# Optimization experiments

Measured on AMD Instinct MI355X. Metric: run time of the kernel, lower is better.

Reference implementation:

```python
import jax, jax.numpy as jnp
import numpy as np

B, N, E, H = 2, 512, 128, 256
IN_DIM = 3 * E + 1


def setup_inputs() -> dict:
    key = jax.random.key(0)
    ks = jax.random.split(key, 9)
    node_embed = jax.random.normal(ks[0], (B, N, E), dtype=jnp.float32)
    problems = jax.random.uniform(ks[1], (B, N, 4), dtype=jnp.float32)
    euclid = jax.random.uniform(ks[2], (B, N, N), dtype=jnp.float32)
    euclid = 0.5 * (euclid + jnp.swapaxes(euclid, 1, 2))  # symmetric, realistic
    s = 0.02
    W1 = s * jax.random.normal(ks[3], (IN_DIM, H), dtype=jnp.float32)
    b1 = jnp.zeros((H,), jnp.float32)
    W2 = s * jax.random.normal(ks[4], (H, H), dtype=jnp.float32)
    b2 = jnp.zeros((H,), jnp.float32)
    W3 = s * jax.random.normal(ks[5], (H, 1), dtype=jnp.float32)
    b3 = jnp.zeros((1,), jnp.float32)
    return {"node_embed": node_embed, "problems": problems,
            "euclid_distance_matrix": euclid,
            "W1": W1, "b1": b1, "W2": W2, "b2": b2, "W3": W3, "b3": b3}


def _forward(node_embed, euclid, W1, b1, W2, b2, W3, b3):
    b, n, e = node_embed.shape
    hi = jnp.broadcast_to(node_embed[:, :, None, :], (b, n, n, e))
    hj = jnp.broadcast_to(node_embed[:, None, :, :], (b, n, n, e))
    habs = jnp.abs(node_embed[:, :, None, :] - node_embed[:, None, :, :])
    x = jnp.concatenate([hi, hj, habs, euclid[..., None]], axis=-1)  # (B,N,N,3E+1)
    h = jax.nn.relu(jnp.einsum('bijf,fh->bijh', x, W1) + b1)
    h = jax.nn.relu(jnp.einsum('bijh,hg->bijg', h, W2) + b2)
    pred = (jnp.einsum('bijh,ho->bijo', h, W3) + b3)[..., 0]  # (B,N,N)
    pred = 0.5 * (pred + jnp.swapaxes(pred, 1, 2))
    pred = pred * (1.0 - jnp.eye(n, dtype=pred.dtype))  # zero diagonal
    return pred


def reference(node_embed, problems, euclid_distance_matrix, W1, b1, W2, b2, W3, b3):
    # euclid_distance_matrix provided, so `problems` fallback path is unused
    return _forward(node_embed, euclid_distance_matrix, W1, b1, W2, b2, W3, b3)
```

## Files before the change

### kernel.cpp

```cpp
#include <hip/hip_runtime.h>
#include <hip/hip_bf16.h>


#define BN 512
#define EE 128
#define HH 256

typedef __attribute__((ext_vector_type(8)))  short short8;
typedef __attribute__((ext_vector_type(16))) float f32x16;
typedef __attribute__((ext_vector_type(4)))  float f32x4;

static __device__ __forceinline__ unsigned short f2bf(float f) {
    __bf16 h = (__bf16)f;
    return __builtin_bit_cast(unsigned short, h);
}
static __device__ __forceinline__ float bf2f(unsigned short s) {
    return (float)__builtin_bit_cast(__bf16, s);
}
static __device__ __forceinline__ f32x16 zero16() {
    f32x16 v;
    #pragma unroll
    for (int i = 0; i < 16; ++i) v[i] = 0.f;
    return v;
}
#define MFMA(a, b, c) __builtin_amdgcn_mfma_f32_32x32x16_bf16((a), (b), (c), 0, 0, 0)

__global__ void pack_all(const float* __restrict__ W1, const float* __restrict__ W2,
                         const float* __restrict__ b2,
                         unsigned short* __restrict__ w1c_p, unsigned short* __restrict__ w1b_p,
                         unsigned short* __restrict__ w2_p,  unsigned short* __restrict__ w1d_f,
                         unsigned short* __restrict__ b2_f) {
    int idx = blockIdx.x * 256 + threadIdx.x;
    {
        int t = idx & 7, l = (idx >> 3) & 63, nb = (idx >> 9) & 7, kb = idx >> 12;
        int k = kb * 16 + (l >> 5) * 8 + t, n = nb * 32 + (l & 31);
        w2_p[idx] = f2bf(W2[k * HH + n]);
        if (idx < 32768) {
            w1c_p[idx] = f2bf(W1[(2 * EE + k) * HH + n]);
            w1b_p[idx] = f2bf(W1[(EE + k) * HH + n]);
        }
    }
    if (idx < 4096) {
        int t = idx & 7, l = (idx >> 3) & 63, nb = idx >> 9;
        int n = nb * 32 + (l & 31);
        bool nz = (t == 0 && l < 32);
        w1d_f[idx] = nz ? f2bf(W1[(3 * EE) * HH + n]) : (unsigned short)0;
        b2_f[idx]  = nz ? f2bf(b2[n]) : (unsigned short)0;
    }
}

__global__ void precompute_pa(const float* __restrict__ node, const float* __restrict__ W1,
                              const float* __restrict__ b1, float* __restrict__ PA) {
    int bi = blockIdx.x, h = threadIdx.x;
    const float* nd = node + (size_t)bi * EE;
    float sa = b1[h];
    #pragma unroll 8
    for (int e = 0; e < EE; ++e) sa += nd[e] * W1[e * HH + h];
    PA[bi * HH + h] = sa;
}

__global__ __launch_bounds__(256, 2) void edge_main(
    const float* __restrict__ node, const float* __restrict__ euclid,
    const float* __restrict__ W3, const float* __restrict__ b3,
    const float* __restrict__ PA,
    const unsigned short* __restrict__ w1c_p, const unsigned short* __restrict__ w1b_p,
    const unsigned short* __restrict__ w2_p,  const unsigned short* __restrict__ w1d_f,
    const unsigned short* __restrict__ b2_f,
    float* __restrict__ out)
{
    __shared__ __align__(16) unsigned short lds_buf[128 * 264];
    __shared__ __align__(16) float hi_f[EE];
    __shared__ float lds_e[128];
    __shared__ float pp[256];

    const int jt = blockIdx.x, i = blockIdx.y, b = blockIdx.z;
    const int jbase = jt * 128;
    const int tid = threadIdx.x, wave = tid >> 6, lane = tid & 63;
    const int m0 = lane & 31, q = lane >> 5, kq = q * 8;
    unsigned short* hjb = lds_buf + 128 * 136;

    if (tid < 32)
        ((f32x4*)hi_f)[tid] = ((const f32x4*)(node + ((size_t)b * BN + i) * EE))[tid];
    if (tid < 128)
        lds_e[tid] = euclid[((size_t)b * BN + i) * BN + jbase + tid];
    __syncthreads();

    {
        int row = tid >> 1, half = tid & 1;
        const f32x4* nj = (const f32x4*)(node + ((size_t)b * BN + jbase + row) * EE);
        const f32x4* hv = (const f32x4*)hi_f;
        int mt = row >> 5, r31 = row & 31;
        #pragma unroll
        for (int g = 0; g < 8; ++g) {
            int c0 = half * 64 + g * 8;
            f32x4 a0 = nj[c0 / 4], a1 = nj[c0 / 4 + 1];
            f32x4 h0 = hv[c0 / 4], h1v = hv[c0 / 4 + 1];
            short8 pd, ph;
            #pragma unroll
            for (int u = 0; u < 4; ++u) {
                pd[u]     = (short)f2bf(fabsf(a0[u] - h0[u]));
                pd[4 + u] = (short)f2bf(fabsf(a1[u] - h1v[u]));
                ph[u]     = (short)f2bf(a0[u]);
                ph[4 + u] = (short)f2bf(a1[u]);
            }
            *(short8*)&lds_buf[row * 136 + c0] = pd;
            int kb = c0 >> 4, hk = (c0 >> 3) & 1;
            *(short8*)&hjb[((mt * 8 + kb) * 64 + r31 + 32 * hk) * 8] = ph;
        }
    }
    __syncthreads();

    f32x16 acc[4][2];
    #pragma unroll
    for (int mt = 0; mt < 4; ++mt) { acc[mt][0] = zero16(); acc[mt][1] = zero16(); }
    {
        const short8* bc  = (const short8*)w1c_p;
        const short8* bb  = (const short8*)w1b_p;
        const short8* hjf = (const short8*)hjb;
        #pragma unroll
        for (int kb = 0; kb < 8; ++kb) {
            short8 b0 = bc[(kb * 8 + wave * 2 + 0) * 64 + lane];
            short8 b1 = bc[(kb * 8 + wave * 2 + 1) * 64 + lane];
            short8 c0 = bb[(kb * 8 + wave * 2 + 0) * 64 + lane];
            short8 c1 = bb[(kb * 8 + wave * 2 + 1) * 64 + lane];
            #pragma unroll
            for (int mt = 0; mt < 4; ++mt) {
                short8 ad = *(const short8*)&lds_buf[(mt * 32 + m0) * 136 + kb * 16 + kq];
                short8 ah = hjf[(mt * 8 + kb) * 64 + lane];
                acc[mt][0] = MFMA(ad, b0, acc[mt][0]);
                acc[mt][1] = MFMA(ad, b1, acc[mt][1]);
                acc[mt][0] = MFMA(ah, c0, acc[mt][0]);
                acc[mt][1] = MFMA(ah, c1, acc[mt][1]);
            }
        }
        short8 d0 = ((const short8*)w1d_f)[(wave * 2 + 0) * 64 + lane];
        short8 d1 = ((const short8*)w1d_f)[(wave * 2 + 1) * 64 + lane];
        #pragma unroll
        for (int mt = 0; mt < 4; ++mt) {
            short8 ae;
            #pragma unroll
            for (int u = 0; u < 8; ++u) ae[u] = 0;
            if (lane < 32) ae[0] = (short)f2bf(lds_e[mt * 32 + m0]);
            acc[mt][0] = MFMA(ae, d0, acc[mt][0]);
            acc[mt][1] = MFMA(ae, d1, acc[mt][1]);
        }
    }
    __syncthreads();

    {
        const float* paRow = PA + ((size_t)b * BN + i) * HH;
        int col0 = wave * 64 + m0;
        float pa0 = paRow[col0], pa1 = paRow[col0 + 32];
        int rq = 4 * q;
        #pragma unroll
        for (int mt = 0; mt < 4; ++mt) {
            #pragma unroll
            for (int r = 0; r < 16; ++r) {
                int row = mt * 32 + (r & 3) + 8 * (r >> 2) + rq;
                float v0 = acc[mt][0][r] + pa0; v0 = v0 > 0.f ? v0 : 0.f;
                float v1 = acc[mt][1][r] + pa1; v1 = v1 > 0.f ? v1 : 0.f;
                lds_buf[row * 264 + col0]      = f2bf(v0);
                lds_buf[row * 264 + col0 + 32] = f2bf(v1);
            }
        }
    }
    __syncthreads();

    f32x16 c2[4][2];
    #pragma unroll
    for (int mt = 0; mt < 4; ++mt) { c2[mt][0] = zero16(); c2[mt][1] = zero16(); }
    {
        const short8* bp = (const short8*)w2_p;
        #pragma unroll
        for (int kb = 0; kb < 16; ++kb) {
            short8 b0 = bp[(kb * 8 + wave * 2 + 0) * 64 + lane];
            short8 b1 = bp[(kb * 8 + wave * 2 + 1) * 64 + lane];
            #pragma unroll
            for (int mt = 0; mt < 4; ++mt) {
                short8 a = *(const short8*)&lds_buf[(mt * 32 + m0) * 264 + kb * 16 + kq];
                c2[mt][0] = MFMA(a, b0, c2[mt][0]);
                c2[mt][1] = MFMA(a, b1, c2[mt][1]);
            }
        }
        short8 aone;
        #pragma unroll
        for (int u = 0; u < 8; ++u) aone[u] = 0;
        if (lane < 32) aone[0] = (short)0x3F80;
        short8 e0 = ((const short8*)b2_f)[(wave * 2 + 0) * 64 + lane];
        short8 e1 = ((const short8*)b2_f)[(wave * 2 + 1) * 64 + lane];
        #pragma unroll
        for (int mt = 0; mt < 4; ++mt) {
            c2[mt][0] = MFMA(aone, e0, c2[mt][0]);
            c2[mt][1] = MFMA(aone, e1, c2[mt][1]);
        }
    }
    __syncthreads();

    {
        int col0 = wave * 64 + m0;
        int rq = 4 * q;
        #pragma unroll
        for (int mt = 0; mt < 4; ++mt) {
            #pragma unroll
            for (int r = 0; r < 16; ++r) {
                int row = mt * 32 + (r & 3) + 8 * (r >> 2) + rq;
                float v0 = c2[mt][0][r] > 0.f ? c2[mt][0][r] : 0.f;
                float v1 = c2[mt][1][r] > 0.f ? c2[mt][1][r] : 0.f;
                lds_buf[row * 264 + col0]      = f2bf(v0);
                lds_buf[row * 264 + col0 + 32] = f2bf(v1);
            }
        }
    }
    __syncthreads();

    {
        int row = tid >> 1, halfc = (tid & 1) * 128;
        float s = 0.f;
        #pragma unroll
        for (int k = 0; k < 16; ++k) {
            short8 h8 = *(const short8*)&lds_buf[row * 264 + halfc + k * 8];
            #pragma unroll
            for (int u = 0; u < 8; ++u)
                s += bf2f((unsigned short)h8[u]) * W3[halfc + k * 8 + u];
        }
        pp[tid] = s;
    }
    __syncthreads();
    if (tid < 128) {
        float v = pp[tid * 2] + pp[tid * 2 + 1] + b3[0];
        out[((size_t)b * BN + i) * BN + jbase + tid] = v;
    }
}

__global__ void symmetrize(float* __restrict__ out) {
    int b = blockIdx.z, ti = blockIdx.y, tj = blockIdx.x;
    if (tj < ti) return;
    int i = ti * 32 + threadIdx.y, j = tj * 32 + threadIdx.x;
    float* p = out + (size_t)b * BN * BN;
    if (i == j) { p[(size_t)i * BN + j] = 0.f; return; }
    if (j < i) return;
    float a = p[(size_t)i * BN + j];
    float c = p[(size_t)j * BN + i];
    float v = 0.5f * (a + c);
    p[(size_t)i * BN + j] = v;
    p[(size_t)j * BN + i] = v;
}

extern "C" void kernel_launch(void* const* d_in, const int* in_sizes, int n_in,
                              void* d_out, int out_size, void* d_ws, size_t ws_size,
                              hipStream_t stream) {
    const float* node   = (const float*)d_in[0];
    const float* euclid = (const float*)d_in[2];
    const float* W1     = (const float*)d_in[3];
    const float* b1     = (const float*)d_in[4];
    const float* W2     = (const float*)d_in[5];
    const float* b2     = (const float*)d_in[6];
    const float* W3     = (const float*)d_in[7];
    const float* b3     = (const float*)d_in[8];
    float* out = (float*)d_out;

    char* ws = (char*)d_ws;
    float*          PA    = (float*)ws;
    unsigned short* w1c_p = (unsigned short*)(ws + (1u << 20));
    unsigned short* w1b_p = (unsigned short*)(ws + (1u << 20) + 65536);
    unsigned short* w2_p  = (unsigned short*)(ws + (1u << 20) + 131072);
    unsigned short* w1d_f = (unsigned short*)(ws + (1u << 20) + 262144);
    unsigned short* b2_f  = (unsigned short*)(ws + (1u << 20) + 270336);

    pack_all<<<256, 256, 0, stream>>>(W1, W2, b2, w1c_p, w1b_p, w2_p, w1d_f, b2_f);
    precompute_pa<<<BN * 2, 256, 0, stream>>>(node, W1, b1, PA);
    edge_main<<<dim3(BN / 128, BN, 2), 256, 0, stream>>>(
        node, euclid, W3, b3, PA, w1c_p, w1b_p, w2_p, w1d_f, b2_f, out);
    symmetrize<<<dim3(BN / 32, BN / 32, 2), dim3(32, 32), 0, stream>>>(out);
}
```

Before: 243.7 us.

## Make edge kernel persistent over tiles with prepacked node operands and shuffle-reduced output layer

Each workgroup now processes eight (b,i,j-tile) tiles in a loop instead of one. The |hi-hj| tile for the next iteration is built while the current one finishes, and the previous tile's output is written at the start of the next iteration. The hj operand is prepacked once into MFMA layout in global memory, and bias b2 is added in registers instead of through an extra MFMA. The final H->1 projection is done with cross-lane shuffle reductions rather than a second LDS write-back and reread. In exchange, launch bounds drop to one workgroup per SIMD occupancy hint, the 64-float partial arrays raise register pressure, and the grid has fewer workgroups.

```diff
diff --git a/kernel.cpp b/kernel.cpp
--- a/kernel.cpp
+++ b/kernel.cpp
@@ -5,6 +5,7 @@
 #define BN 512
 #define EE 128
 #define HH 256
+#define TILES_PER_WG 8
 
 typedef __attribute__((ext_vector_type(8)))  short short8;
 typedef __attribute__((ext_vector_type(16))) float f32x16;
@@ -13,9 +14,6 @@
 static __device__ __forceinline__ unsigned short f2bf(float f) {
     __bf16 h = (__bf16)f;
     return __builtin_bit_cast(unsigned short, h);
-}
-static __device__ __forceinline__ float bf2f(unsigned short s) {
-    return (float)__builtin_bit_cast(__bf16, s);
 }
 static __device__ __forceinline__ f32x16 zero16() {
     f32x16 v;
@@ -25,13 +23,19 @@
 }
 #define MFMA(a, b, c) __builtin_amdgcn_mfma_f32_32x32x16_bf16((a), (b), (c), 0, 0, 0)
 
-__global__ void pack_all(const float* __restrict__ W1, const float* __restrict__ W2,
-                         const float* __restrict__ b2,
+__global__ void pack_all(const float* __restrict__ node, const float* __restrict__ W1,
+                         const float* __restrict__ W2,
                          unsigned short* __restrict__ w1c_p, unsigned short* __restrict__ w1b_p,
                          unsigned short* __restrict__ w2_p,  unsigned short* __restrict__ w1d_f,
-                         unsigned short* __restrict__ b2_f) {
+                         unsigned short* __restrict__ node_p) {
     int idx = blockIdx.x * 256 + threadIdx.x;
     {
+        int t = idx & 7, l = (idx >> 3) & 63, kb = (idx >> 9) & 7;
+        int j32 = (idx >> 12) & 15, b = (idx >> 16) & 1;
+        int j = j32 * 32 + (l & 31), e = kb * 16 + (l >> 5) * 8 + t;
+        node_p[idx] = f2bf(node[((size_t)b * BN + j) * EE + e]);
+    }
+    if (idx < 65536) {
         int t = idx & 7, l = (idx >> 3) & 63, nb = (idx >> 9) & 7, kb = idx >> 12;
         int k = kb * 16 + (l >> 5) * 8 + t, n = nb * 32 + (l & 31);
         w2_p[idx] = f2bf(W2[k * HH + n]);
@@ -45,7 +49,6 @@
         int n = nb * 32 + (l & 31);
         bool nz = (t == 0 && l < 32);
         w1d_f[idx] = nz ? f2bf(W1[(3 * EE) * HH + n]) : (unsigned short)0;
-        b2_f[idx]  = nz ? f2bf(b2[n]) : (unsigned short)0;
     }
 }
 
@@ -59,176 +62,181 @@
     PA[bi * HH + h] = sa;
 }
 
-__global__ __launch_bounds__(256, 2) void edge_main(
+__global__ __launch_bounds__(256, 1) void edge_main(
     const float* __restrict__ node, const float* __restrict__ euclid,
     const float* __restrict__ W3, const float* __restrict__ b3,
-    const float* __restrict__ PA,
+    const float* __restrict__ b2v, const float* __restrict__ PA,
     const unsigned short* __restrict__ w1c_p, const unsigned short* __restrict__ w1b_p,
     const unsigned short* __restrict__ w2_p,  const unsigned short* __restrict__ w1d_f,
-    const unsigned short* __restrict__ b2_f,
+    const unsigned short* __restrict__ node_p,
     float* __restrict__ out)
 {
-    __shared__ __align__(16) unsigned short lds_buf[128 * 264];
-    __shared__ __align__(16) float hi_f[EE];
-    __shared__ float lds_e[128];
-    __shared__ float pp[256];
-
-    const int jt = blockIdx.x, i = blockIdx.y, b = blockIdx.z;
-    const int jbase = jt * 128;
+    __shared__ __align__(16) unsigned short lds_D[128 * 136];
+    __shared__ __align__(16) unsigned short lds_h1[128 * 264];
+    __shared__ float pp[512];
+
+    const int wg = blockIdx.x;
     const int tid = threadIdx.x, wave = tid >> 6, lane = tid & 63;
     const int m0 = lane & 31, q = lane >> 5, kq = q * 8;
-    unsigned short* hjb = lds_buf + 128 * 136;
-
-    if (tid < 32)
-        ((f32x4*)hi_f)[tid] = ((const f32x4*)(node + ((size_t)b * BN + i) * EE))[tid];
-    if (tid < 128)
-        lds_e[tid] = euclid[((size_t)b * BN + i) * BN + jbase + tid];
-    __syncthreads();
-
-    {
+    const int col0 = wave * 64 + m0;
+
+    const float w30 = W3[col0], w31 = W3[col0 + 32];
+    const float b20 = b2v[col0], b21 = b2v[col0 + 32];
+    const float b3v = b3[0];
+    const short8 d0 = ((const short8*)w1d_f)[(wave * 2 + 0) * 64 + lane];
+    const short8 d1 = ((const short8*)w1d_f)[(wave * 2 + 1) * 64 + lane];
+
+    auto buildD = [&](int g) {
+        int b = g >> 11, i = (g >> 2) & 511, jbase = (g & 3) * 128;
         int row = tid >> 1, half = tid & 1;
         const f32x4* nj = (const f32x4*)(node + ((size_t)b * BN + jbase + row) * EE);
-        const f32x4* hv = (const f32x4*)hi_f;
-        int mt = row >> 5, r31 = row & 31;
+        const f32x4* hv = (const f32x4*)(node + ((size_t)b * BN + i) * EE);
+        unsigned short* dst = &lds_D[row * 136 + half * 64];
         #pragma unroll
-        for (int g = 0; g < 8; ++g) {
-            int c0 = half * 64 + g * 8;
-            f32x4 a0 = nj[c0 / 4], a1 = nj[c0 / 4 + 1];
-            f32x4 h0 = hv[c0 / 4], h1v = hv[c0 / 4 + 1];
-            short8 pd, ph;
+        for (int gg = 0; gg < 8; ++gg) {
+            int c0 = half * 16 + gg * 2;
+            f32x4 a0 = nj[c0], a1 = nj[c0 + 1];
+            f32x4 h0 = hv[c0], h1v = hv[c0 + 1];
+            short8 pd;
             #pragma unroll
             for (int u = 0; u < 4; ++u) {
                 pd[u]     = (short)f2bf(fabsf(a0[u] - h0[u]));
                 pd[4 + u] = (short)f2bf(fabsf(a1[u] - h1v[u]));
-                ph[u]     = (short)f2bf(a0[u]);
-                ph[4 + u] = (short)f2bf(a1[u]);
-            }
-            *(short8*)&lds_buf[row * 136 + c0] = pd;
-            int kb = c0 >> 4, hk = (c0 >> 3) & 1;
-            *(short8*)&hjb[((mt * 8 + kb) * 64 + r31 + 32 * hk) * 8] = ph;
-        }
-    }
+            }
+            *(short8*)(dst + gg * 8) = pd;
+        }
+    };
+
+    buildD(wg * TILES_PER_WG);
     __syncthreads();
 
-    f32x16 acc[4][2];
-    #pragma unroll
-    for (int mt = 0; mt < 4; ++mt) { acc[mt][0] = zero16(); acc[mt][1] = zero16(); }
+    #pragma unroll 1
+    for (int t = 0; t < TILES_PER_WG; ++t) {
+        const int g = wg * TILES_PER_WG + t;
+        const int b = g >> 11, i = (g >> 2) & 511, jbase = (g & 3) * 128;
+
+        if (t > 0 && tid < 128) {
+            const int gp = g - 1;
+            int bp = gp >> 11, ip = (gp >> 2) & 511, jp = gp & 3;
+            float v = pp[tid] + pp[128 + tid] + pp[256 + tid] + pp[384 + tid] + b3v;
+            out[((size_t)bp * BN + ip) * BN + jp * 128 + tid] = v;
+        }
+
+        f32x16 acc[4][2];
+        #pragma unroll
+        for (int mt = 0; mt < 4; ++mt) { acc[mt][0] = zero16(); acc[mt][1] = zero16(); }
+        {
+            const short8* bc = (const short8*)w1c_p;
+            const short8* bb = (const short8*)w1b_p;
+            const short8* np = (const short8*)node_p;
+            const int npb = b * 128 + (g & 3) * 32;
+            #pragma unroll
+            for (int kb = 0; kb < 8; ++kb) {
+                short8 b0 = bc[(kb * 8 + wave * 2 + 0) * 64 + lane];
+                short8 b1 = bc[(kb * 8 + wave * 2 + 1) * 64 + lane];
+                short8 c0 = bb[(kb * 8 + wave * 2 + 0) * 64 + lane];
+                short8 c1 = bb[(kb * 8 + wave * 2 + 1) * 64 + lane];
+                #pragma unroll
+                for (int mt = 0; mt < 4; ++mt) {
+                    short8 ad = *(const short8*)&lds_D[(mt * 32 + m0) * 136 + kb * 16 + kq];
+                    short8 ah = np[(npb + mt * 8 + kb) * 64 + lane];
+                    acc[mt][0] = MFMA(ad, b0, acc[mt][0]);
+                    acc[mt][1] = MFMA(ad, b1, acc[mt][1]);
+                    acc[mt][0] = MFMA(ah, c0, acc[mt][0]);
+                    acc[mt][1] = MFMA(ah, c1, acc[mt][1]);
+                }
+            }
+            const float* erow = euclid + ((size_t)b * BN + i) * BN + jbase;
+            #pragma unroll
+            for (int mt = 0; mt < 4; ++mt) {
+                short8 ae;
+                #pragma unroll
+                for (int u = 0; u < 8; ++u) ae[u] = 0;
+                if (lane < 32) ae[0] = (short)f2bf(erow[mt * 32 + m0]);
+                acc[mt][0] = MFMA(ae, d0, acc[mt][0]);
+                acc[mt][1] = MFMA(ae, d1, acc[mt][1]);
+            }
+        }
+        {
+            const float* paRow = PA + ((size_t)b * BN + i) * HH;
+            float pa0 = paRow[col0], pa1 = paRow[col0 + 32];
+            int rq = 4 * q;
+            #pragma unroll
+            for (int mt = 0; mt < 4; ++mt) {
+                #pragma unroll
+                for (int r = 0; r < 16; ++r) {
+                    int row = mt * 32 + (r & 3) + 8 * (r >> 2) + rq;
+                    float v0 = acc[mt][0][r] + pa0; v0 = v0 > 0.f ? v0 : 0.f;
+                    float v1 = acc[mt][1][r] + pa1; v1 = v1 > 0.f ? v1 : 0.f;
+                    lds_h1[row * 264 + col0]      = f2bf(v0);
+                    lds_h1[row * 264 + col0 + 32] = f2bf(v1);
+                }
+            }
+        }
+        __syncthreads();
+
+        f32x16 c2[4][2];
+        #pragma unroll
+        for (int mt = 0; mt < 4; ++mt) { c2[mt][0] = zero16(); c2[mt][1] = zero16(); }
+        {
+            const short8* bp = (const short8*)w2_p;
+            #pragma unroll
+            for (int kb = 0; kb < 16; ++kb) {
+                short8 b0 = bp[(kb * 8 + wave * 2 + 0) * 64 + lane];
+                short8 b1 = bp[(kb * 8 + wave * 2 + 1) * 64 + lane];
+                #pragma unroll
+                for (int mt = 0; mt < 4; ++mt) {
+                    short8 a = *(const short8*)&lds_h1[(mt * 32 + m0) * 264 + kb * 16 + kq];
+                    c2[mt][0] = MFMA(a, b0, c2[mt][0]);
+                    c2[mt][1] = MFMA(a, b1, c2[mt][1]);
+                }
+            }
+        }
+        {
+            float part[64];
+            #pragma unroll
+            for (int mt = 0; mt < 4; ++mt) {
+                #pragma unroll
+                for (int r = 0; r < 16; ++r) {
+                    float h2a = c2[mt][0][r] + b20; h2a = h2a > 0.f ? h2a : 0.f;
+                    float h2b = c2[mt][1][r] + b21; h2b = h2b > 0.f ? h2b : 0.f;
+                    part[mt * 16 + r] = h2a * w30 + h2b * w31;
+                }
+            }
+            int cnt = 32;
+            #pragma unroll
+            for (int lvl = 0; lvl < 5; ++lvl) {
+                int m = 1 << lvl;
+                #pragma unroll
+                for (int j = 0; j < cnt; ++j) {
+                    bool up = (lane & m) != 0;
+                    float send = up ? part[j] : part[j + cnt];
+                    float keep = up ? part[j + cnt] : part[j];
+                    part[j] = keep + __shfl_xor(send, m, 64);
+                }
+                cnt >>= 1;
+            }
+            int base = (lane & 1) * 32 + ((lane >> 1) & 1) * 16 + ((lane >> 2) & 1) * 8
+                     + ((lane >> 3) & 1) * 4 + ((lane >> 4) & 1) * 2;
+            #pragma unroll
+            for (int which = 0; which < 2; ++which) {
+                int jr = base + which;
+                int mt = jr >> 4, r = jr & 15;
+                int row = mt * 32 + (r & 3) + 8 * (r >> 2) + 4 * q;
+                pp[wave * 128 + row] = part[which];
+            }
+        }
+        if (t + 1 < TILES_PER_WG) buildD(g + 1);
+        __syncthreads();
+    }
+
     {
-        const short8* bc  = (const short8*)w1c_p;
-        const short8* bb  = (const short8*)w1b_p;
-        const short8* hjf = (const short8*)hjb;
-        #pragma unroll
-        for (int kb = 0; kb < 8; ++kb) {
-            short8 b0 = bc[(kb * 8 + wave * 2 + 0) * 64 + lane];
-            short8 b1 = bc[(kb * 8 + wave * 2 + 1) * 64 + lane];
-            short8 c0 = bb[(kb * 8 + wave * 2 + 0) * 64 + lane];
-            short8 c1 = bb[(kb * 8 + wave * 2 + 1) * 64 + lane];
-            #pragma unroll
-            for (int mt = 0; mt < 4; ++mt) {
-                short8 ad = *(const short8*)&lds_buf[(mt * 32 + m0) * 136 + kb * 16 + kq];
-                short8 ah = hjf[(mt * 8 + kb) * 64 + lane];
-                acc[mt][0] = MFMA(ad, b0, acc[mt][0]);
-                acc[mt][1] = MFMA(ad, b1, acc[mt][1]);
-                acc[mt][0] = MFMA(ah, c0, acc[mt][0]);
-                acc[mt][1] = MFMA(ah, c1, acc[mt][1]);
-            }
-        }
-        short8 d0 = ((const short8*)w1d_f)[(wave * 2 + 0) * 64 + lane];
-        short8 d1 = ((const short8*)w1d_f)[(wave * 2 + 1) * 64 + lane];
-        #pragma unroll
-        for (int mt = 0; mt < 4; ++mt) {
-            short8 ae;
-            #pragma unroll
-            for (int u = 0; u < 8; ++u) ae[u] = 0;
-            if (lane < 32) ae[0] = (short)f2bf(lds_e[mt * 32 + m0]);
-            acc[mt][0] = MFMA(ae, d0, acc[mt][0]);
-            acc[mt][1] = MFMA(ae, d1, acc[mt][1]);
-        }
-    }
-    __syncthreads();
-
-    {
-        const float* paRow = PA + ((size_t)b * BN + i) * HH;
-        int col0 = wave * 64 + m0;
-        float pa0 = paRow[col0], pa1 = paRow[col0 + 32];
-        int rq = 4 * q;
-        #pragma unroll
-        for (int mt = 0; mt < 4; ++mt) {
-            #pragma unroll
-            for (int r = 0; r < 16; ++r) {
-                int row = mt * 32 + (r & 3) + 8 * (r >> 2) + rq;
-                float v0 = acc[mt][0][r] + pa0; v0 = v0 > 0.f ? v0 : 0.f;
-                float v1 = acc[mt][1][r] + pa1; v1 = v1 > 0.f ? v1 : 0.f;
-                lds_buf[row * 264 + col0]      = f2bf(v0);
-                lds_buf[row * 264 + col0 + 32] = f2bf(v1);
-            }
-        }
-    }
-    __syncthreads();
-
-    f32x16 c2[4][2];
-    #pragma unroll
-    for (int mt = 0; mt < 4; ++mt) { c2[mt][0] = zero16(); c2[mt][1] = zero16(); }
-    {
-        const short8* bp = (const short8*)w2_p;
-        #pragma unroll
-        for (int kb = 0; kb < 16; ++kb) {
-            short8 b0 = bp[(kb * 8 + wave * 2 + 0) * 64 + lane];
-            short8 b1 = bp[(kb * 8 + wave * 2 + 1) * 64 + lane];
-            #pragma unroll
-            for (int mt = 0; mt < 4; ++mt) {
-                short8 a = *(const short8*)&lds_buf[(mt * 32 + m0) * 264 + kb * 16 + kq];
-                c2[mt][0] = MFMA(a, b0, c2[mt][0]);
-                c2[mt][1] = MFMA(a, b1, c2[mt][1]);
-            }
-        }
-        short8 aone;
-        #pragma unroll
-        for (int u = 0; u < 8; ++u) aone[u] = 0;
-        if (lane < 32) aone[0] = (short)0x3F80;
-        short8 e0 = ((const short8*)b2_f)[(wave * 2 + 0) * 64 + lane];
-        short8 e1 = ((const short8*)b2_f)[(wave * 2 + 1) * 64 + lane];
-        #pragma unroll
-        for (int mt = 0; mt < 4; ++mt) {
-            c2[mt][0] = MFMA(aone, e0, c2[mt][0]);
-            c2[mt][1] = MFMA(aone, e1, c2[mt][1]);
-        }
-    }
-    __syncthreads();
-
-    {
-        int col0 = wave * 64 + m0;
-        int rq = 4 * q;
-        #pragma unroll
-        for (int mt = 0; mt < 4; ++mt) {
-            #pragma unroll
-            for (int r = 0; r < 16; ++r) {
-                int row = mt * 32 + (r & 3) + 8 * (r >> 2) + rq;
-                float v0 = c2[mt][0][r] > 0.f ? c2[mt][0][r] : 0.f;
-                float v1 = c2[mt][1][r] > 0.f ? c2[mt][1][r] : 0.f;
-                lds_buf[row * 264 + col0]      = f2bf(v0);
-                lds_buf[row * 264 + col0 + 32] = f2bf(v1);
-            }
-        }
-    }
-    __syncthreads();
-
-    {
-        int row = tid >> 1, halfc = (tid & 1) * 128;
-        float s = 0.f;
-        #pragma unroll
-        for (int k = 0; k < 16; ++k) {
-            short8 h8 = *(const short8*)&lds_buf[row * 264 + halfc + k * 8];
-            #pragma unroll
-            for (int u = 0; u < 8; ++u)
-                s += bf2f((unsigned short)h8[u]) * W3[halfc + k * 8 + u];
-        }
-        pp[tid] = s;
-    }
-    __syncthreads();
-    if (tid < 128) {
-        float v = pp[tid * 2] + pp[tid * 2 + 1] + b3[0];
-        out[((size_t)b * BN + i) * BN + jbase + tid] = v;
+        const int gp = wg * TILES_PER_WG + TILES_PER_WG - 1;
+        int bp = gp >> 11, ip = (gp >> 2) & 511, jp = gp & 3;
+        if (tid < 128) {
+            float v = pp[tid] + pp[128 + tid] + pp[256 + tid] + pp[384 + tid] + b3v;
+            out[((size_t)bp * BN + ip) * BN + jp * 128 + tid] = v;
+        }
     }
 }
 
@@ -260,16 +268,16 @@
     float* out = (float*)d_out;
 
     char* ws = (char*)d_ws;
-    float*          PA    = (float*)ws;
-    unsigned short* w1c_p = (unsigned short*)(ws + (1u << 20));
-    unsigned short* w1b_p = (unsigned short*)(ws + (1u << 20) + 65536);
-    unsigned short* w2_p  = (unsigned short*)(ws + (1u << 20) + 131072);
-    unsigned short* w1d_f = (unsigned short*)(ws + (1u << 20) + 262144);
-    unsigned short* b2_f  = (unsigned short*)(ws + (1u << 20) + 270336);
-
-    pack_all<<<256, 256, 0, stream>>>(W1, W2, b2, w1c_p, w1b_p, w2_p, w1d_f, b2_f);
+    float*          PA     = (float*)ws;
+    unsigned short* w1c_p  = (unsigned short*)(ws + (1u << 20));
+    unsigned short* w1b_p  = (unsigned short*)(ws + (1u << 20) + 65536);
+    unsigned short* w2_p   = (unsigned short*)(ws + (1u << 20) + 131072);
+    unsigned short* w1d_f  = (unsigned short*)(ws + (1u << 20) + 262144);
+    unsigned short* node_p = (unsigned short*)(ws + (1u << 20) + 270336);
+
+    pack_all<<<512, 256, 0, stream>>>(node, W1, W2, w1c_p, w1b_p, w2_p, w1d_f, node_p);
     precompute_pa<<<BN * 2, 256, 0, stream>>>(node, W1, b1, PA);
-    edge_main<<<dim3(BN / 128, BN, 2), 256, 0, stream>>>(
-        node, euclid, W3, b3, PA, w1c_p, w1b_p, w2_p, w1d_f, b2_f, out);
+    edge_main<<<(BN / 128) * BN * 2 / TILES_PER_WG, 256, 0, stream>>>(
+        node, euclid, W3, b3, b2, PA, w1c_p, w1b_p, w2_p, w1d_f, node_p, out);
     symmetrize<<<dim3(BN / 32, BN / 32, 2), dim3(32, 32), 0, stream>>>(out);
 }
```

Result: slower. 366.7 us (+50.5%).

## Prepack node embeddings to bf16 MFMA layout and merge prep kernels

Applied to the files above, without the earlier changes.

Adds a node_p buffer holding node embeddings already converted to bf16 in MFMA operand order. The edge kernel now reads its hj operand straight from global memory instead of converting and staging it in LDS per block. The hi and euclid staging arrays and the first barrier are removed, with those values read directly from global memory. The pack and PA-precompute kernels are merged into one launch to cut launch overhead, at the cost of more global and cache traffic in the main loop.

```diff
diff --git a/kernel.cpp b/kernel.cpp
--- a/kernel.cpp
+++ b/kernel.cpp
@@ -25,38 +25,46 @@
 }
 #define MFMA(a, b, c) __builtin_amdgcn_mfma_f32_32x32x16_bf16((a), (b), (c), 0, 0, 0)
 
-__global__ void pack_all(const float* __restrict__ W1, const float* __restrict__ W2,
-                         const float* __restrict__ b2,
-                         unsigned short* __restrict__ w1c_p, unsigned short* __restrict__ w1b_p,
-                         unsigned short* __restrict__ w2_p,  unsigned short* __restrict__ w1d_f,
-                         unsigned short* __restrict__ b2_f) {
-    int idx = blockIdx.x * 256 + threadIdx.x;
-    {
-        int t = idx & 7, l = (idx >> 3) & 63, nb = (idx >> 9) & 7, kb = idx >> 12;
-        int k = kb * 16 + (l >> 5) * 8 + t, n = nb * 32 + (l & 31);
-        w2_p[idx] = f2bf(W2[k * HH + n]);
-        if (idx < 32768) {
-            w1c_p[idx] = f2bf(W1[(2 * EE + k) * HH + n]);
-            w1b_p[idx] = f2bf(W1[(EE + k) * HH + n]);
-        }
-    }
-    if (idx < 4096) {
-        int t = idx & 7, l = (idx >> 3) & 63, nb = idx >> 9;
-        int n = nb * 32 + (l & 31);
-        bool nz = (t == 0 && l < 32);
-        w1d_f[idx] = nz ? f2bf(W1[(3 * EE) * HH + n]) : (unsigned short)0;
-        b2_f[idx]  = nz ? f2bf(b2[n]) : (unsigned short)0;
-    }
-}
-
-__global__ void precompute_pa(const float* __restrict__ node, const float* __restrict__ W1,
-                              const float* __restrict__ b1, float* __restrict__ PA) {
-    int bi = blockIdx.x, h = threadIdx.x;
-    const float* nd = node + (size_t)bi * EE;
-    float sa = b1[h];
-    #pragma unroll 8
-    for (int e = 0; e < EE; ++e) sa += nd[e] * W1[e * HH + h];
-    PA[bi * HH + h] = sa;
+__global__ void prep(const float* __restrict__ node, const float* __restrict__ W1,
+                     const float* __restrict__ W2, const float* __restrict__ b1,
+                     const float* __restrict__ b2, float* __restrict__ PA,
+                     unsigned short* __restrict__ w1c_p, unsigned short* __restrict__ w1b_p,
+                     unsigned short* __restrict__ w2_p,  unsigned short* __restrict__ w1d_f,
+                     unsigned short* __restrict__ b2_f,  unsigned short* __restrict__ node_p) {
+    int blk = blockIdx.x;
+    if (blk < 512) {
+        int idx = blk * 256 + threadIdx.x;
+        {
+            int t = idx & 7, l = (idx >> 3) & 63, kb = (idx >> 9) & 7;
+            int j32 = (idx >> 12) & 15, b = (idx >> 16) & 1;
+            int j = j32 * 32 + (l & 31), e = kb * 16 + (l >> 5) * 8 + t;
+            node_p[idx] = f2bf(node[((size_t)b * BN + j) * EE + e]);
+        }
+        if (idx < 65536) {
+            int t = idx & 7, l = (idx >> 3) & 63, nb = (idx >> 9) & 7, kb = idx >> 12;
+            int k = kb * 16 + (l >> 5) * 8 + t, n = nb * 32 + (l & 31);
+            w2_p[idx] = f2bf(W2[k * HH + n]);
+            if (idx < 32768) {
+                w1c_p[idx] = f2bf(W1[(2 * EE + k) * HH + n]);
+                w1b_p[idx] = f2bf(W1[(EE + k) * HH + n]);
+            }
+        }
+        if (idx < 4096) {
+            int t = idx & 7, l = (idx >> 3) & 63, nb = idx >> 9;
+            int n = nb * 32 + (l & 31);
+            bool nz = (t == 0 && l < 32);
+            w1d_f[idx] = nz ? f2bf(W1[(3 * EE) * HH + n]) : (unsigned short)0;
+            b2_f[idx]  = nz ? f2bf(b2[n]) : (unsigned short)0;
+        }
+    } else {
+        int bi = blk - 512;
+        int h = threadIdx.x;
+        const float* nd = node + (size_t)bi * EE;
+        float sa = b1[h];
+        #pragma unroll 8
+        for (int e = 0; e < EE; ++e) sa += nd[e] * W1[e * HH + h];
+        PA[bi * HH + h] = sa;
+    }
 }
 
 __global__ __launch_bounds__(256, 2) void edge_main(
@@ -65,47 +73,35 @@
     const float* __restrict__ PA,
     const unsigned short* __restrict__ w1c_p, const unsigned short* __restrict__ w1b_p,
     const unsigned short* __restrict__ w2_p,  const unsigned short* __restrict__ w1d_f,
-    const unsigned short* __restrict__ b2_f,
+    const unsigned short* __restrict__ b2_f,  const unsigned short* __restrict__ node_p,
     float* __restrict__ out)
 {
     __shared__ __align__(16) unsigned short lds_buf[128 * 264];
-    __shared__ __align__(16) float hi_f[EE];
-    __shared__ float lds_e[128];
     __shared__ float pp[256];
 
     const int jt = blockIdx.x, i = blockIdx.y, b = blockIdx.z;
     const int jbase = jt * 128;
     const int tid = threadIdx.x, wave = tid >> 6, lane = tid & 63;
     const int m0 = lane & 31, q = lane >> 5, kq = q * 8;
-    unsigned short* hjb = lds_buf + 128 * 136;
-
-    if (tid < 32)
-        ((f32x4*)hi_f)[tid] = ((const f32x4*)(node + ((size_t)b * BN + i) * EE))[tid];
-    if (tid < 128)
-        lds_e[tid] = euclid[((size_t)b * BN + i) * BN + jbase + tid];
-    __syncthreads();
+    const int col0 = wave * 64 + m0;
 
     {
         int row = tid >> 1, half = tid & 1;
         const f32x4* nj = (const f32x4*)(node + ((size_t)b * BN + jbase + row) * EE);
-        const f32x4* hv = (const f32x4*)hi_f;
-        int mt = row >> 5, r31 = row & 31;
+        const f32x4* hv = (const f32x4*)(node + ((size_t)b * BN + i) * EE);
+        unsigned short* dst = &lds_buf[row * 136 + half * 64];
         #pragma unroll
         for (int g = 0; g < 8; ++g) {
-            int c0 = half * 64 + g * 8;
-            f32x4 a0 = nj[c0 / 4], a1 = nj[c0 / 4 + 1];
-            f32x4 h0 = hv[c0 / 4], h1v = hv[c0 / 4 + 1];
-            short8 pd, ph;
+            int c0 = half * 16 + g * 2;
+            f32x4 a0 = nj[c0], a1 = nj[c0 + 1];
+            f32x4 h0 = hv[c0], h1v = hv[c0 + 1];
+            short8 pd;
             #pragma unroll
             for (int u = 0; u < 4; ++u) {
                 pd[u]     = (short)f2bf(fabsf(a0[u] - h0[u]));
                 pd[4 + u] = (short)f2bf(fabsf(a1[u] - h1v[u]));
-                ph[u]     = (short)f2bf(a0[u]);
-                ph[4 + u] = (short)f2bf(a1[u]);
-            }
-            *(short8*)&lds_buf[row * 136 + c0] = pd;
-            int kb = c0 >> 4, hk = (c0 >> 3) & 1;
-            *(short8*)&hjb[((mt * 8 + kb) * 64 + r31 + 32 * hk) * 8] = ph;
+            }
+            *(short8*)(dst + g * 8) = pd;
         }
     }
     __syncthreads();
@@ -114,9 +110,10 @@
     #pragma unroll
     for (int mt = 0; mt < 4; ++mt) { acc[mt][0] = zero16(); acc[mt][1] = zero16(); }
     {
-        const short8* bc  = (const short8*)w1c_p;
-        const short8* bb  = (const short8*)w1b_p;
-        const short8* hjf = (const short8*)hjb;
+        const short8* bc = (const short8*)w1c_p;
+        const short8* bb = (const short8*)w1b_p;
+        const short8* np = (const short8*)node_p;
+        const int npb = b * 128 + jt * 32;
         #pragma unroll
         for (int kb = 0; kb < 8; ++kb) {
             short8 b0 = bc[(kb * 8 + wave * 2 + 0) * 64 + lane];
@@ -126,13 +123,14 @@
             #pragma unroll
             for (int mt = 0; mt < 4; ++mt) {
                 short8 ad = *(const short8*)&lds_buf[(mt * 32 + m0) * 136 + kb * 16 + kq];
-                short8 ah = hjf[(mt * 8 + kb) * 64 + lane];
+                short8 ah = np[(npb + mt * 8 + kb) * 64 + lane];
                 acc[mt][0] = MFMA(ad, b0, acc[mt][0]);
                 acc[mt][1] = MFMA(ad, b1, acc[mt][1]);
                 acc[mt][0] = MFMA(ah, c0, acc[mt][0]);
                 acc[mt][1] = MFMA(ah, c1, acc[mt][1]);
             }
         }
+        const float* erow = euclid + ((size_t)b * BN + i) * BN + jbase;
         short8 d0 = ((const short8*)w1d_f)[(wave * 2 + 0) * 64 + lane];
         short8 d1 = ((const short8*)w1d_f)[(wave * 2 + 1) * 64 + lane];
         #pragma unroll
@@ -140,7 +138,7 @@
             short8 ae;
             #pragma unroll
             for (int u = 0; u < 8; ++u) ae[u] = 0;
-            if (lane < 32) ae[0] = (short)f2bf(lds_e[mt * 32 + m0]);
+            if (lane < 32) ae[0] = (short)f2bf(erow[mt * 32 + m0]);
             acc[mt][0] = MFMA(ae, d0, acc[mt][0]);
             acc[mt][1] = MFMA(ae, d1, acc[mt][1]);
         }
@@ -149,7 +147,6 @@
 
     {
         const float* paRow = PA + ((size_t)b * BN + i) * HH;
-        int col0 = wave * 64 + m0;
         float pa0 = paRow[col0], pa1 = paRow[col0 + 32];
         int rq = 4 * q;
         #pragma unroll
@@ -197,7 +194,6 @@
     __syncthreads();
 
     {
-        int col0 = wave * 64 + m0;
         int rq = 4 * q;
         #pragma unroll
         for (int mt = 0; mt < 4; ++mt) {
@@ -260,16 +256,17 @@
     float* out = (float*)d_out;
 
     char* ws = (char*)d_ws;
-    float*          PA    = (float*)ws;
-    unsigned short* w1c_p = (unsigned short*)(ws + (1u << 20));
-    unsigned short* w1b_p = (unsigned short*)(ws + (1u << 20) + 65536);
-    unsigned short* w2_p  = (unsigned short*)(ws + (1u << 20) + 131072);
-    unsigned short* w1d_f = (unsigned short*)(ws + (1u << 20) + 262144);
-    unsigned short* b2_f  = (unsigned short*)(ws + (1u << 20) + 270336);
-
-    pack_all<<<256, 256, 0, stream>>>(W1, W2, b2, w1c_p, w1b_p, w2_p, w1d_f, b2_f);
-    precompute_pa<<<BN * 2, 256, 0, stream>>>(node, W1, b1, PA);
+    float*          PA     = (float*)ws;
+    unsigned short* w1c_p  = (unsigned short*)(ws + (1u << 20));
+    unsigned short* w1b_p  = (unsigned short*)(ws + (1u << 20) + 65536);
+    unsigned short* w2_p   = (unsigned short*)(ws + (1u << 20) + 131072);
+    unsigned short* w1d_f  = (unsigned short*)(ws + (1u << 20) + 262144);
+    unsigned short* b2_f   = (unsigned short*)(ws + (1u << 20) + 270336);
+    unsigned short* node_p = (unsigned short*)(ws + (1u << 20) + 278528);
+
+    prep<<<1536, 256, 0, stream>>>(node, W1, W2, b1, b2, PA,
+                                   w1c_p, w1b_p, w2_p, w1d_f, b2_f, node_p);
     edge_main<<<dim3(BN / 128, BN, 2), 256, 0, stream>>>(
-        node, euclid, W3, b3, PA, w1c_p, w1b_p, w2_p, w1d_f, b2_f, out);
+        node, euclid, W3, b3, PA, w1c_p, w1b_p, w2_p, w1d_f, b2_f, node_p, out);
     symmetrize<<<dim3(BN / 32, BN / 32, 2), dim3(32, 32), 0, stream>>>(out);
 }
```

Result: slower. 268.3 us (+10.1%).
